# Kernel tuning notes

Hardware: AMD Instinct MI355X
Metric: run time of the kernel (lower is better)

## Reference

```python
import jax, jax.numpy as jnp
import numpy as np

N_HEADS = 16

def setup_inputs() -> dict:
    key = jax.random.key(0)
    k0, k1, k2 = jax.random.split(key, 3)
    B, T, C = 4, 2048, 1024
    x = jax.random.normal(k0, (B, T, C), dtype=jnp.float32)
    # nn.Linear params: y = x @ W.T + b
    w_qkv = jax.random.normal(k1, (3 * C, C), dtype=jnp.float32) * 0.02
    b_qkv = jnp.zeros((3 * C,), dtype=jnp.float32)
    w_proj = jax.random.normal(k2, (C, C), dtype=jnp.float32) * 0.02
    b_proj = jnp.zeros((C,), dtype=jnp.float32)
    return {"x": x, "w_qkv": w_qkv, "b_qkv": b_qkv, "w_proj": w_proj, "b_proj": b_proj}

def reference(x, w_qkv, b_qkv, w_proj, b_proj):
    B, T, C = x.shape
    H = N_HEADS
    hd = C // H
    qkv = x @ w_qkv.T + b_qkv                      # [B, T, 3C]
    q, k, v = jnp.split(qkv, 3, axis=-1)           # each [B, T, C]
    q = q.reshape(B, T, H, hd).transpose(0, 2, 1, 3)  # [B, H, T, hd]
    k = k.reshape(B, T, H, hd).transpose(0, 2, 1, 3)
    v = v.reshape(B, T, H, hd).transpose(0, 2, 1, 3)
    # note: original scales by emb_dim**-0.5 (C), not head_dim**-0.5
    wei = jnp.einsum("bhqd,bhkd->bhqk", q, k) * (C ** -0.5)  # [B, H, T, T]
    causal = jnp.tril(jnp.ones((T, T), dtype=bool))
    wei = jnp.where(causal, wei, -jnp.inf)
    att = jax.nn.softmax(wei, axis=-1)
    out = jnp.einsum("bhqk,bhkd->bhqd", att, v)    # [B, H, T, hd]
    out = out.transpose(0, 2, 1, 3).reshape(B, T, C)
    return out @ w_proj.T + b_proj
```

## Files before the change

kernel.cpp:

```cpp
#include <hip/hip_runtime.h>
#include <hip/hip_bf16.h>

typedef __bf16 bf16;
typedef __bf16 bf16x8 __attribute__((ext_vector_type(8)));
typedef __bf16 bf16x4 __attribute__((ext_vector_type(4)));
typedef float  f32x4  __attribute__((ext_vector_type(4)));

#define LDS_ASYNC16(g, l)                                            \
  __builtin_amdgcn_global_load_lds(                                  \
      (const __attribute__((address_space(1))) void*)(g),            \
      (__attribute__((address_space(3))) void*)(l), 16, 0, 0)

#define QSCALE 0.04508421995f

template <int CTRL>
__device__ __forceinline__ float dpp_mov(float x) {
  return __builtin_bit_cast(
      float, __builtin_amdgcn_update_dpp(0, __builtin_bit_cast(int, x), CTRL,
                                         0xf, 0xf, true));
}
__device__ __forceinline__ float red_sum16(float x) {
  x += dpp_mov<0xB1>(x);
  x += dpp_mov<0x4E>(x);
  x += dpp_mov<0x141>(x);
  x += dpp_mov<0x140>(x);
  return x;
}

__global__ void cvt_f32_bf16(const float* __restrict__ in,
                             bf16* __restrict__ out, int n4) {
  int i = blockIdx.x * blockDim.x + threadIdx.x;
  if (i >= n4) return;
  float4 v = ((const float4*)in)[i];
  bf16x4 o = {(bf16)v.x, (bf16)v.y, (bf16)v.z, (bf16)v.w};
  ((bf16x4*)out)[i] = o;
}

template <int MODE>
__global__ __launch_bounds__(256) void gemm_bt(
    const bf16* __restrict__ A, const bf16* __restrict__ B,
    const float* __restrict__ bias, float* __restrict__ outf,
    bf16* __restrict__ oq, bf16* __restrict__ ok, bf16* __restrict__ ov,
    int M, int N, int K) {
  __shared__ bf16 As[128 * 32];
  __shared__ bf16 Bs[128 * 32];
  const int tid = threadIdx.x;
  const int wave = tid >> 6, lane = tid & 63;
  const int quad = lane >> 4, l15 = lane & 15;
  const int bm = blockIdx.x * 128, bn = blockIdx.y * 128;
  const int wrow = (wave >> 1) << 6, wcol = (wave & 1) << 6;
  const int srow = tid >> 2;
  const int schunk = (tid & 3) * 8;

  f32x4 acc[4][4] = {};

  const bf16* ga0 = A + (size_t)(bm + srow) * K + schunk;
  const bf16* ga1 = A + (size_t)(bm + srow + 64) * K + schunk;
  const bf16* gb0 = B + (size_t)(bn + srow) * K + schunk;
  const bf16* gb1 = B + (size_t)(bn + srow + 64) * K + schunk;
  char* lA = (char*)As + wave * 1024;
  char* lB = (char*)Bs + wave * 1024;

  for (int k0 = 0; k0 < K; k0 += 32) {
    __syncthreads();
    LDS_ASYNC16(ga0 + k0, lA);
    LDS_ASYNC16(ga1 + k0, lA + 4096);
    LDS_ASYNC16(gb0 + k0, lB);
    LDS_ASYNC16(gb1 + k0, lB + 4096);
    __syncthreads();
    bf16x8 af[4], bfr[4];
#pragma unroll
    for (int mi = 0; mi < 4; ++mi)
      af[mi] = *(const bf16x8*)&As[(wrow + mi * 16 + l15) * 32 + quad * 8];
#pragma unroll
    for (int ni = 0; ni < 4; ++ni)
      bfr[ni] = *(const bf16x8*)&Bs[(wcol + ni * 16 + l15) * 32 + quad * 8];
#pragma unroll
    for (int mi = 0; mi < 4; ++mi)
#pragma unroll
      for (int ni = 0; ni < 4; ++ni)
        acc[mi][ni] = __builtin_amdgcn_mfma_f32_16x16x32_bf16(
            af[mi], bfr[ni], acc[mi][ni], 0, 0, 0);
  }

#pragma unroll
  for (int mi = 0; mi < 4; ++mi) {
    const int row0 = bm + wrow + mi * 16 + quad * 4;
#pragma unroll
    for (int ni = 0; ni < 4; ++ni) {
      const int col = bn + wcol + ni * 16 + l15;
      const float bv = bias[col];
      if (MODE == 0) {
#pragma unroll
        for (int r = 0; r < 4; ++r)
          outf[(size_t)(row0 + r) * N + col] = acc[mi][ni][r] + bv;
      } else {
        const int part = col >> 10;
        const int cn = col & 1023, h = cn >> 6, d = cn & 63;
        const int b = row0 >> 11, t0 = row0 & 2047;
        if (part == 2) {
          bf16x4 pk = {(bf16)(acc[mi][ni][0] + bv), (bf16)(acc[mi][ni][1] + bv),
                       (bf16)(acc[mi][ni][2] + bv), (bf16)(acc[mi][ni][3] + bv)};
          *(bf16x4*)(ov + ((size_t)(b * 16 + h) * 64 + d) * 2048 + t0) = pk;
        } else {
          const float sc = part ? 1.0f : QSCALE;
          bf16* dst = (part ? ok : oq) + ((size_t)(b * 16 + h) * 2048 + t0) * 64 + d;
#pragma unroll
          for (int r = 0; r < 4; ++r)
            dst[(size_t)r * 64] = (bf16)((acc[mi][ni][r] + bv) * sc);
        }
      }
    }
  }
}

__global__ __launch_bounds__(256) void flash_attn(
    const bf16* __restrict__ qb, const bf16* __restrict__ kb,
    const bf16* __restrict__ vt, bf16* __restrict__ ob) {
  constexpr int T = 2048;
  __shared__ bf16 Ks[64 * 72];
  __shared__ bf16 Vs[64 * 72];
  __shared__ bf16 Ps[4][32 * 72];
  const int tid = threadIdx.x, wave = tid >> 6, lane = tid & 63;
  const int quad = lane >> 4, l15 = lane & 15;
  const int bh = blockIdx.x;
  const int b = bh >> 4, h = bh & 15;
  const bf16* qbase = qb + (size_t)bh * T * 64;
  const bf16* kbase = kb + (size_t)bh * T * 64;
  const bf16* vbase = vt + (size_t)bh * 64 * T;
  const int srow = tid >> 3, sc = (tid & 7) * 8;

#pragma unroll 1
  for (int half = 0; half < 2; ++half) {
    const int qt = half ? (15 - (int)blockIdx.y) : (int)blockIdx.y;
    const int q0 = qt * 128 + wave * 32;

    bf16x8 qf[2][2];
#pragma unroll
    for (int mi = 0; mi < 2; ++mi)
#pragma unroll
      for (int ks = 0; ks < 2; ++ks)
        qf[mi][ks] = *(const bf16x8*)(qbase + (size_t)(q0 + mi * 16 + l15) * 64 +
                                      ks * 32 + quad * 8);

    f32x4 lsum[2] = {};
    f32x4 oacc[2][4] = {};

    const int nkt = 2 * qt + 2;
    const int ktp = q0 >> 6;
#pragma unroll 1
    for (int kt = 0; kt < nkt; ++kt) {
      __syncthreads();
#pragma unroll
      for (int p = 0; p < 2; ++p) {
        const int r = srow + p * 32;
        *(uint4*)&Ks[r * 72 + sc] =
            *(const uint4*)(kbase + (size_t)(kt * 64 + r) * 64 + sc);
        *(uint4*)&Vs[r * 72 + sc] =
            *(const uint4*)(vbase + (size_t)r * T + kt * 64 + sc);
      }
      __syncthreads();
      if (kt <= ktp) {
        f32x4 s[2][4];
        bf16x8 kf[4][2];
#pragma unroll
        for (int ni = 0; ni < 4; ++ni)
#pragma unroll
          for (int ks = 0; ks < 2; ++ks)
            kf[ni][ks] =
                *(const bf16x8*)&Ks[(ni * 16 + l15) * 72 + ks * 32 + quad * 8];
#pragma unroll
        for (int mi = 0; mi < 2; ++mi)
#pragma unroll
          for (int ni = 0; ni < 4; ++ni) {
            f32x4 a = {0.f, 0.f, 0.f, 0.f};
            a = __builtin_amdgcn_mfma_f32_16x16x32_bf16(qf[mi][0], kf[ni][0], a, 0, 0, 0);
            a = __builtin_amdgcn_mfma_f32_16x16x32_bf16(qf[mi][1], kf[ni][1], a, 0, 0, 0);
            s[mi][ni] = a;
          }
        if (kt == ktp) {
#pragma unroll
          for (int mi = 0; mi < 2; ++mi)
#pragma unroll
            for (int ni = 0; ni < 4; ++ni)
#pragma unroll
              for (int r = 0; r < 4; ++r) {
                const int qrow = q0 + mi * 16 + quad * 4 + r;
                const int kcol = kt * 64 + ni * 16 + l15;
                if (kcol > qrow) s[mi][ni][r] = -__builtin_inff();
              }
        }
#pragma unroll
        for (int mi = 0; mi < 2; ++mi)
#pragma unroll
          for (int ni = 0; ni < 4; ++ni) {
#pragma unroll
            for (int r = 0; r < 4; ++r)
              s[mi][ni][r] = __builtin_amdgcn_exp2f(s[mi][ni][r]);
            lsum[mi] += s[mi][ni];
          }
#pragma unroll
        for (int mi = 0; mi < 2; ++mi)
#pragma unroll
          for (int ni = 0; ni < 4; ++ni)
#pragma unroll
            for (int r = 0; r < 4; ++r)
              Ps[wave][(mi * 16 + quad * 4 + r) * 72 + ni * 16 + l15] =
                  (bf16)s[mi][ni][r];
        bf16x8 pf[2][2], vf[4][2];
#pragma unroll
        for (int mi = 0; mi < 2; ++mi)
#pragma unroll
          for (int ks = 0; ks < 2; ++ks)
            pf[mi][ks] = *(const bf16x8*)&Ps[wave][(mi * 16 + l15) * 72 +
                                                   ks * 32 + quad * 8];
#pragma unroll
        for (int di = 0; di < 4; ++di)
#pragma unroll
          for (int ks = 0; ks < 2; ++ks)
            vf[di][ks] =
                *(const bf16x8*)&Vs[(di * 16 + l15) * 72 + ks * 32 + quad * 8];
#pragma unroll
        for (int mi = 0; mi < 2; ++mi)
#pragma unroll
          for (int di = 0; di < 4; ++di) {
            oacc[mi][di] = __builtin_amdgcn_mfma_f32_16x16x32_bf16(
                pf[mi][0], vf[di][0], oacc[mi][di], 0, 0, 0);
            oacc[mi][di] = __builtin_amdgcn_mfma_f32_16x16x32_bf16(
                pf[mi][1], vf[di][1], oacc[mi][di], 0, 0, 0);
          }
      }
    }
#pragma unroll
    for (int mi = 0; mi < 2; ++mi)
#pragma unroll
      for (int r = 0; r < 4; ++r) {
        const float l = red_sum16(lsum[mi][r]);
        const float inv = 1.f / l;
        const int t = q0 + mi * 16 + quad * 4 + r;
#pragma unroll
        for (int di = 0; di < 4; ++di) {
          const int d = di * 16 + l15;
          ob[((size_t)b * 2048 + t) * 1024 + h * 64 + d] =
              (bf16)(oacc[mi][di][r] * inv);
        }
      }
  }
}

extern "C" void kernel_launch(void* const* d_in, const int* in_sizes, int n_in,
                              void* d_out, int out_size, void* d_ws,
                              size_t ws_size, hipStream_t stream) {
  const float* x = (const float*)d_in[0];
  const float* w_qkv = (const float*)d_in[1];
  const float* b_qkv = (const float*)d_in[2];
  const float* w_proj = (const float*)d_in[3];
  const float* b_proj = (const float*)d_in[4];
  float* out = (float*)d_out;

  const int B = 4, T = 2048, C = 1024;
  const size_t nx = (size_t)B * T * C;

  char* ws = (char*)d_ws;
  bf16* xb = (bf16*)ws;      ws += nx * 2;
  bf16* wqkvb = (bf16*)ws;   ws += (size_t)3 * C * C * 2;
  bf16* wprojb = (bf16*)ws;  ws += (size_t)C * C * 2;
  bf16* qb = (bf16*)ws;      ws += nx * 2;
  bf16* kbuf = (bf16*)ws;    ws += nx * 2;
  bf16* vtb = (bf16*)ws;     ws += nx * 2;
  bf16* attb = (bf16*)ws;    ws += nx * 2;

  cvt_f32_bf16<<<(int)(nx / 4 / 256), 256, 0, stream>>>(x, xb, (int)(nx / 4));
  cvt_f32_bf16<<<3 * C * C / 4 / 256, 256, 0, stream>>>(w_qkv, wqkvb, 3 * C * C / 4);
  cvt_f32_bf16<<<C * C / 4 / 256, 256, 0, stream>>>(w_proj, wprojb, C * C / 4);

  dim3 g1(64, 24);
  gemm_bt<1><<<g1, 256, 0, stream>>>(xb, wqkvb, b_qkv, nullptr, qb, kbuf, vtb,
                                     B * T, 3 * C, C);
  dim3 g2(64, 8);
  flash_attn<<<g2, 256, 0, stream>>>(qb, kbuf, vtb, attb);

  dim3 g3(64, 8);
  gemm_bt<0><<<g3, 256, 0, stream>>>(attb, wprojb, b_proj, out, nullptr,
                                     nullptr, nullptr, B * T, C, C);
}
```

Measured before the change: 283.2 us.

## Double-buffer K/V tiles and keep P in registers via transposed S

Double-buffers the K and V LDS tiles, issuing global loads for the next tile before the compute on the current one and storing them afterwards, which drops one barrier per iteration. It computes S transposed (K as the A operand) so the exp'd probabilities land in a layout that feeds the 16x16x16 bf16 MFMA directly from registers, removing the per-wave Ps LDS round trip. The row-sum reduction moves from DPP to a small LDS exchange. The cost is more registers held across compute and twice as many smaller-K MFMAs for PV. There is a possible hazard in the final Ls write and read with no barrier, though it stays within a single wave.

```diff
diff --git a/kernel.cpp b/kernel.cpp
--- a/kernel.cpp
+++ b/kernel.cpp
@@ -5,6 +5,7 @@
 typedef __bf16 bf16x8 __attribute__((ext_vector_type(8)));
 typedef __bf16 bf16x4 __attribute__((ext_vector_type(4)));
 typedef float  f32x4  __attribute__((ext_vector_type(4)));
+typedef short  short4_t __attribute__((ext_vector_type(4)));
 
 #define LDS_ASYNC16(g, l)                                            \
   __builtin_amdgcn_global_load_lds(                                  \
@@ -12,20 +13,6 @@
       (__attribute__((address_space(3))) void*)(l), 16, 0, 0)
 
 #define QSCALE 0.04508421995f
-
-template <int CTRL>
-__device__ __forceinline__ float dpp_mov(float x) {
-  return __builtin_bit_cast(
-      float, __builtin_amdgcn_update_dpp(0, __builtin_bit_cast(int, x), CTRL,
-                                         0xf, 0xf, true));
-}
-__device__ __forceinline__ float red_sum16(float x) {
-  x += dpp_mov<0xB1>(x);
-  x += dpp_mov<0x4E>(x);
-  x += dpp_mov<0x141>(x);
-  x += dpp_mov<0x140>(x);
-  return x;
-}
 
 __global__ void cvt_f32_bf16(const float* __restrict__ in,
                              bf16* __restrict__ out, int n4) {
@@ -118,9 +105,9 @@
     const bf16* __restrict__ qb, const bf16* __restrict__ kb,
     const bf16* __restrict__ vt, bf16* __restrict__ ob) {
   constexpr int T = 2048;
-  __shared__ bf16 Ks[64 * 72];
-  __shared__ bf16 Vs[64 * 72];
-  __shared__ bf16 Ps[4][32 * 72];
+  __shared__ bf16 Ks[2][64 * 72];
+  __shared__ bf16 Vs[2][64 * 72];
+  __shared__ float Ls[4][2][4][16];
   const int tid = threadIdx.x, wave = tid >> 6, lane = tid & 63;
   const int quad = lane >> 4, l15 = lane & 15;
   const int bh = blockIdx.x;
@@ -137,112 +124,123 @@
 
     bf16x8 qf[2][2];
 #pragma unroll
-    for (int mi = 0; mi < 2; ++mi)
+    for (int qi = 0; qi < 2; ++qi)
 #pragma unroll
       for (int ks = 0; ks < 2; ++ks)
-        qf[mi][ks] = *(const bf16x8*)(qbase + (size_t)(q0 + mi * 16 + l15) * 64 +
+        qf[qi][ks] = *(const bf16x8*)(qbase + (size_t)(q0 + qi * 16 + l15) * 64 +
                                       ks * 32 + quad * 8);
 
-    f32x4 lsum[2] = {};
+    f32x4 lsumv[2] = {};
     f32x4 oacc[2][4] = {};
 
     const int nkt = 2 * qt + 2;
     const int ktp = q0 >> 6;
+
+    {
+      uint4 k0 = *(const uint4*)(kbase + (size_t)srow * 64 + sc);
+      uint4 k1 = *(const uint4*)(kbase + (size_t)(srow + 32) * 64 + sc);
+      uint4 v0 = *(const uint4*)(vbase + (size_t)srow * T + sc);
+      uint4 v1 = *(const uint4*)(vbase + (size_t)(srow + 32) * T + sc);
+      *(uint4*)&Ks[0][srow * 72 + sc] = k0;
+      *(uint4*)&Ks[0][(srow + 32) * 72 + sc] = k1;
+      *(uint4*)&Vs[0][srow * 72 + sc] = v0;
+      *(uint4*)&Vs[0][(srow + 32) * 72 + sc] = v1;
+    }
+
 #pragma unroll 1
     for (int kt = 0; kt < nkt; ++kt) {
       __syncthreads();
-#pragma unroll
-      for (int p = 0; p < 2; ++p) {
-        const int r = srow + p * 32;
-        *(uint4*)&Ks[r * 72 + sc] =
-            *(const uint4*)(kbase + (size_t)(kt * 64 + r) * 64 + sc);
-        *(uint4*)&Vs[r * 72 + sc] =
-            *(const uint4*)(vbase + (size_t)r * T + kt * 64 + sc);
-      }
-      __syncthreads();
+      const int cur = kt & 1;
+      const bool pre = (kt + 1) < nkt;
+      uint4 pk0, pk1, pv0, pv1;
+      if (pre) {
+        const bf16* kp = kbase + (size_t)(kt + 1) * 64 * 64;
+        const bf16* vp = vbase + (kt + 1) * 64;
+        pk0 = *(const uint4*)(kp + (size_t)srow * 64 + sc);
+        pk1 = *(const uint4*)(kp + (size_t)(srow + 32) * 64 + sc);
+        pv0 = *(const uint4*)(vp + (size_t)srow * T + sc);
+        pv1 = *(const uint4*)(vp + (size_t)(srow + 32) * T + sc);
+      }
       if (kt <= ktp) {
-        f32x4 s[2][4];
-        bf16x8 kf[4][2];
-#pragma unroll
-        for (int ni = 0; ni < 4; ++ni)
-#pragma unroll
-          for (int ks = 0; ks < 2; ++ks)
-            kf[ni][ks] =
-                *(const bf16x8*)&Ks[(ni * 16 + l15) * 72 + ks * 32 + quad * 8];
-#pragma unroll
-        for (int mi = 0; mi < 2; ++mi)
-#pragma unroll
-          for (int ni = 0; ni < 4; ++ni) {
+        f32x4 st[4][2];
+#pragma unroll
+        for (int ki = 0; ki < 4; ++ki) {
+          bf16x8 kfa = *(const bf16x8*)&Ks[cur][(ki * 16 + l15) * 72 + quad * 8];
+          bf16x8 kfb =
+              *(const bf16x8*)&Ks[cur][(ki * 16 + l15) * 72 + 32 + quad * 8];
+#pragma unroll
+          for (int qi = 0; qi < 2; ++qi) {
             f32x4 a = {0.f, 0.f, 0.f, 0.f};
-            a = __builtin_amdgcn_mfma_f32_16x16x32_bf16(qf[mi][0], kf[ni][0], a, 0, 0, 0);
-            a = __builtin_amdgcn_mfma_f32_16x16x32_bf16(qf[mi][1], kf[ni][1], a, 0, 0, 0);
-            s[mi][ni] = a;
+            a = __builtin_amdgcn_mfma_f32_16x16x32_bf16(kfa, qf[qi][0], a, 0, 0, 0);
+            a = __builtin_amdgcn_mfma_f32_16x16x32_bf16(kfb, qf[qi][1], a, 0, 0, 0);
+            st[ki][qi] = a;
           }
+        }
         if (kt == ktp) {
 #pragma unroll
-          for (int mi = 0; mi < 2; ++mi)
-#pragma unroll
-            for (int ni = 0; ni < 4; ++ni)
+          for (int ki = 0; ki < 4; ++ki)
+#pragma unroll
+            for (int qi = 0; qi < 2; ++qi)
 #pragma unroll
               for (int r = 0; r < 4; ++r) {
-                const int qrow = q0 + mi * 16 + quad * 4 + r;
-                const int kcol = kt * 64 + ni * 16 + l15;
-                if (kcol > qrow) s[mi][ni][r] = -__builtin_inff();
+                const int kcol = kt * 64 + ki * 16 + quad * 4 + r;
+                const int qrow = q0 + qi * 16 + l15;
+                if (kcol > qrow) st[ki][qi][r] = -__builtin_inff();
               }
         }
-#pragma unroll
-        for (int mi = 0; mi < 2; ++mi)
-#pragma unroll
-          for (int ni = 0; ni < 4; ++ni) {
+        short4_t pa[4][2];
+#pragma unroll
+        for (int ki = 0; ki < 4; ++ki)
+#pragma unroll
+          for (int qi = 0; qi < 2; ++qi) {
 #pragma unroll
             for (int r = 0; r < 4; ++r)
-              s[mi][ni][r] = __builtin_amdgcn_exp2f(s[mi][ni][r]);
-            lsum[mi] += s[mi][ni];
+              st[ki][qi][r] = __builtin_amdgcn_exp2f(st[ki][qi][r]);
+            lsumv[qi] += st[ki][qi];
+            bf16x4 pk = {(bf16)st[ki][qi][0], (bf16)st[ki][qi][1],
+                         (bf16)st[ki][qi][2], (bf16)st[ki][qi][3]};
+            pa[ki][qi] = __builtin_bit_cast(short4_t, pk);
           }
 #pragma unroll
-        for (int mi = 0; mi < 2; ++mi)
-#pragma unroll
-          for (int ni = 0; ni < 4; ++ni)
-#pragma unroll
-            for (int r = 0; r < 4; ++r)
-              Ps[wave][(mi * 16 + quad * 4 + r) * 72 + ni * 16 + l15] =
-                  (bf16)s[mi][ni][r];
-        bf16x8 pf[2][2], vf[4][2];
-#pragma unroll
-        for (int mi = 0; mi < 2; ++mi)
-#pragma unroll
-          for (int ks = 0; ks < 2; ++ks)
-            pf[mi][ks] = *(const bf16x8*)&Ps[wave][(mi * 16 + l15) * 72 +
-                                                   ks * 32 + quad * 8];
-#pragma unroll
         for (int di = 0; di < 4; ++di)
 #pragma unroll
-          for (int ks = 0; ks < 2; ++ks)
-            vf[di][ks] =
-                *(const bf16x8*)&Vs[(di * 16 + l15) * 72 + ks * 32 + quad * 8];
-#pragma unroll
-        for (int mi = 0; mi < 2; ++mi)
-#pragma unroll
-          for (int di = 0; di < 4; ++di) {
-            oacc[mi][di] = __builtin_amdgcn_mfma_f32_16x16x32_bf16(
-                pf[mi][0], vf[di][0], oacc[mi][di], 0, 0, 0);
-            oacc[mi][di] = __builtin_amdgcn_mfma_f32_16x16x32_bf16(
-                pf[mi][1], vf[di][1], oacc[mi][di], 0, 0, 0);
+          for (int ki = 0; ki < 4; ++ki) {
+            bf16x4 vv = *(const bf16x4*)&Vs[cur][(di * 16 + l15) * 72 +
+                                               ki * 16 + quad * 4];
+            short4_t vb = __builtin_bit_cast(short4_t, vv);
+#pragma unroll
+            for (int qi = 0; qi < 2; ++qi)
+              oacc[qi][di] = __builtin_amdgcn_mfma_f32_16x16x16bf16_1k(
+                  pa[ki][qi], vb, oacc[qi][di], 0, 0, 0);
           }
       }
+      if (pre) {
+        const int nxt = cur ^ 1;
+        *(uint4*)&Ks[nxt][srow * 72 + sc] = pk0;
+        *(uint4*)&Ks[nxt][(srow + 32) * 72 + sc] = pk1;
+        *(uint4*)&Vs[nxt][srow * 72 + sc] = pv0;
+        *(uint4*)&Vs[nxt][(srow + 32) * 72 + sc] = pv1;
+      }
     }
-#pragma unroll
-    for (int mi = 0; mi < 2; ++mi)
+
+#pragma unroll
+    for (int qi = 0; qi < 2; ++qi)
+      Ls[wave][qi][quad][l15] =
+          lsumv[qi][0] + lsumv[qi][1] + lsumv[qi][2] + lsumv[qi][3];
+#pragma unroll
+    for (int qi = 0; qi < 2; ++qi)
 #pragma unroll
       for (int r = 0; r < 4; ++r) {
-        const float l = red_sum16(lsum[mi][r]);
+        const int rloc = quad * 4 + r;
+        const float l = Ls[wave][qi][0][rloc] + Ls[wave][qi][1][rloc] +
+                        Ls[wave][qi][2][rloc] + Ls[wave][qi][3][rloc];
         const float inv = 1.f / l;
-        const int t = q0 + mi * 16 + quad * 4 + r;
+        const int t = q0 + qi * 16 + rloc;
 #pragma unroll
         for (int di = 0; di < 4; ++di) {
           const int d = di * 16 + l15;
           ob[((size_t)b * 2048 + t) * 1024 + h * 64 + d] =
-              (bf16)(oacc[mi][di][r] * inv);
+              (bf16)(oacc[qi][di][r] * inv);
         }
       }
   }
```

Result: faster. 263.9 us (-6.8%).
